# Kernel tuning notes

Hardware: AMD Instinct MI355X
Metric: run time of the kernel (lower is better)

## Reference

```python
import jax, jax.numpy as jnp
import numpy as np

HEAD = 128
E = 1536
MAXPOS = 2048

def _rope_tables(seq_len, d):
    # get_sinusoid_encoding_table: col 2i = sin(pos/10000^(2i/d)), col 2i+1 = cos(same)
    pos = np.arange(seq_len, dtype=np.float32)[:, None]
    i = np.arange(d // 2, dtype=np.float32)
    ang = pos / np.power(10000.0, 2.0 * i / d)  # [seq, d/2]
    cos_pos = np.repeat(np.cos(ang), 2, axis=-1)  # table[:,1::2] repeat_interleave(2)
    sin_pos = np.repeat(np.sin(ang), 2, axis=-1)  # table[:,0::2] repeat_interleave(2)
    return jnp.asarray(cos_pos), jnp.asarray(sin_pos)

def _apply_rope(x, cos_pos, sin_pos):
    # x: [b, s, d]; rotate pairs (x0,x1) -> (-x1, x0)
    x2 = jnp.stack([-x[..., 1::2], x[..., ::2]], axis=-1).reshape(x.shape)
    return x * cos_pos + x2 * sin_pos

def setup_inputs() -> dict:
    key = jax.random.key(0)
    ks = jax.random.split(key, 6)
    b, s, h = 4, 2048, 768
    return {
        "hidden_states": jax.random.normal(ks[0], (b, s, h), jnp.float32),
        "attention_mask": jnp.ones((b, 1, 1, s), jnp.float32),
        "Wi": jax.random.normal(ks[1], (h, 2 * E + HEAD), jnp.float32) * 0.02,
        "bi": jnp.zeros((2 * E + HEAD,), jnp.float32),
        "gamma": 1.0 + jax.random.normal(ks[2], (2, HEAD), jnp.float32) * 0.02,
        "beta": jnp.zeros((2, HEAD), jnp.float32),
        "Wo": jax.random.normal(ks[3], (E, h), jnp.float32) * 0.02,
        "bo": jnp.zeros((h,), jnp.float32),
    }

def reference(hidden_states, attention_mask, Wi, bi, gamma, beta, Wo, bo):
    b, s, _ = hidden_states.shape
    x = jax.nn.silu(hidden_states @ Wi + bi)  # hidden_act='swish'
    u, v, qk = jnp.split(x, [E, 2 * E], axis=-1)  # [b,s,E],[b,s,E],[b,s,HEAD]
    # OffsetScale with 2 heads -> q, k
    q = qk * gamma[0] + beta[0]
    k = qk * gamma[1] + beta[1]
    cos_pos, sin_pos = _rope_tables(s, HEAD)
    q = _apply_rope(q, cos_pos, sin_pos)
    k = _apply_rope(k, cos_pos, sin_pos)
    scores = jnp.einsum('bid,bjd->bij', q, k) / jnp.sqrt(jnp.float32(HEAD))
    add_mask = (1.0 - attention_mask) * -1e12  # [b,1,1,s]
    scores = scores + jnp.squeeze(add_mask, axis=1)  # broadcast [b,1,s]
    # softmax_plus normalization
    valid = (scores > -1e11).astype(scores.dtype)
    l = jnp.maximum(jnp.sum(valid, axis=-1, keepdims=True), 1.0)
    scale = jnp.log(l) / jnp.log(jnp.float32(512.0))
    attn = jax.nn.softmax(scores * scale, axis=-1)
    out = (u * jnp.einsum('bij,bjd->bid', attn, v)) @ Wo + bo
    return out
```

## Files before the change

### kernel.cpp

```cpp
#include <hip/hip_runtime.h>
#include <math.h>

typedef _Float16 f16;
typedef _Float16 f16x8 __attribute__((ext_vector_type(8)));
typedef float f32x4 __attribute__((ext_vector_type(4)));

#define HEAD 128
#define EDIM 1536
#define NI   3200
#define NIP  3328
#define HDIM 768
#define BATCH 4
#define SEQ  2048
#define MTOT (BATCH*SEQ)

__device__ __forceinline__ void gld_lds16(const void* g, void* l) {
  __builtin_amdgcn_global_load_lds(
      (const __attribute__((address_space(1))) void*)g,
      (__attribute__((address_space(3))) void*)l, 16, 0, 0);
}

__global__ __launch_bounds__(256) void cast_f32_f16_k(const float* __restrict__ in,
                                                      f16* __restrict__ out, int n4) {
  int i = blockIdx.x * 256 + threadIdx.x;
  if (i >= n4) return;
  float4 x = ((const float4*)in)[i];
  union { f16 h[4]; short4 s; } u;
  u.h[0] = (f16)x.x; u.h[1] = (f16)x.y; u.h[2] = (f16)x.z; u.h[3] = (f16)x.w;
  ((short4*)out)[i] = u.s;
}

__global__ __launch_bounds__(256) void transpose_cast_k(const float* __restrict__ in, int ld_in,
                                                        f16* __restrict__ out, int ld_out) {
  __shared__ float tile[32][33];
  int c = threadIdx.x & 31, r0 = threadIdx.x >> 5;
  int ib = blockIdx.y * 32, jb = blockIdx.x * 32;
#pragma unroll
  for (int rr = 0; rr < 32; rr += 8)
    tile[r0 + rr][c] = in[(size_t)(ib + r0 + rr) * ld_in + jb + c];
  __syncthreads();
#pragma unroll
  for (int rr = 0; rr < 32; rr += 8)
    out[(size_t)(jb + r0 + rr) * ld_out + ib + c] = (f16)tile[c][r0 + rr];
}

__global__ __launch_bounds__(256) void rope_tables_k(float* __restrict__ cosT,
                                                     float* __restrict__ sinT) {
  int id = blockIdx.x * 256 + threadIdx.x;
  int pos = id >> 6, i = id & 63;
  float ang = (float)pos / powf(10000.0f, (float)(2 * i) / 128.0f);
  float cv = cosf(ang), sv = sinf(ang);
  cosT[pos * HEAD + 2 * i]     = cv;
  cosT[pos * HEAD + 2 * i + 1] = cv;
  sinT[pos * HEAD + 2 * i]     = sv;
  sinT[pos * HEAD + 2 * i + 1] = sv;
}

__global__ __launch_bounds__(256) void addmask_k(const float* __restrict__ mask,
                                                 float* __restrict__ am) {
  int i = blockIdx.x * 256 + threadIdx.x;
  am[i] = (1.0f - mask[i]) * -1e12f;
}

__global__ __launch_bounds__(256) void rope_gate_k(const f16* __restrict__ qkraw,
                                                   const float* __restrict__ gamma,
                                                   const float* __restrict__ beta,
                                                   const float* __restrict__ cosT,
                                                   const float* __restrict__ sinT,
                                                   f16* __restrict__ Qh,
                                                   f16* __restrict__ Kh) {
  int id = blockIdx.x * 256 + threadIdx.x;
  int row = id >> 4, c0i = (id & 15) * 8;
  int pos = row & (SEQ - 1);
  f16x8 sv8 = *(const f16x8*)(qkraw + (size_t)row * HEAD + c0i);
  f16 oq[8], ok[8];
#pragma unroll
  for (int e = 0; e < 8; e += 2) {
    int c = c0i + e;
    float cs = cosT[pos * HEAD + c], sn = sinT[pos * HEAD + c];
    float s0 = (float)sv8[e], s1 = (float)sv8[e + 1];
    float q0 = s0 * gamma[c] + beta[c];
    float q1 = s1 * gamma[c + 1] + beta[c + 1];
    oq[e]     = (f16)(q0 * cs - q1 * sn);
    oq[e + 1] = (f16)(q1 * cs + q0 * sn);
    float k0 = s0 * gamma[128 + c] + beta[128 + c];
    float k1 = s1 * gamma[128 + c + 1] + beta[128 + c + 1];
    ok[e]     = (f16)(k0 * cs - k1 * sn);
    ok[e + 1] = (f16)(k1 * cs + k0 * sn);
  }
  *(f16x8*)(Qh + (size_t)row * HEAD + c0i) = *(f16x8*)oq;
  *(f16x8*)(Kh + (size_t)row * HEAD + c0i) = *(f16x8*)ok;
}

template <int MODE>
__global__ __launch_bounds__(512, 2)
void gemm8p(const f16* __restrict__ A, int lda,
            const f16* __restrict__ B0, int ldb, long long sB, int bshift, int K,
            f16* __restrict__ outH, f16* __restrict__ outH2,
            f16* __restrict__ outV,
            const float* __restrict__ c0, const f16* __restrict__ hA) {
  __shared__ f16 LS[2][2][2][2][4096];
  int bx, by;
  {
    int gx = gridDim.x;
    int id = blockIdx.y * gx + blockIdx.x;
    int cpx = (gx * gridDim.y) >> 3;
    int sw = (id & 7) * cpx + (id >> 3);
    bx = sw % gx; by = sw / gx;
  }
  const int m0 = by * 256, n0 = bx * 256;
  const int t = threadIdx.x;
  const int lane = t & 63, w = t >> 6;
  const int wr = w >> 2, wc = w & 3;
  const int lr = lane & 15, kg = lane >> 4;
  const int bb = by >> bshift;
  const f16* Bb = B0 + (size_t)bb * sB;

  const int rb = t >> 3;
  const int sl = ((t & 7) ^ (rb & 7)) << 3;
  const f16* gA = A  + (size_t)(m0 + rb) * lda + sl;
  const f16* gB = Bb + (size_t)(n0 + rb) * ldb + sl;
  char* lA = (char*)LS + w * 1024;
  char* lB = (char*)LS + 32768 + w * 1024;

  auto stageA = [&](int kt, int h) {
    const f16* s = gA + (size_t)(h << 7) * lda + (kt << 6);
    char* d = lA + ((kt & 1) << 16) + (h << 14);
    gld_lds16(s, d);
    gld_lds16(s + ((size_t)lda << 6), d + 8192);
  };
  auto stageB = [&](int kt, int h) {
    const f16* s = gB + (size_t)(h << 7) * ldb + (kt << 6);
    char* d = lB + ((kt & 1) << 16) + (h << 14);
    gld_lds16(s, d);
    gld_lds16(s + ((size_t)ldb << 6), d + 8192);
  };

  const char* RA = (const char*)LS + ((wr * 128 + lr) << 7);
  const char* RB = (const char*)LS + 32768 + ((wc * 64 + lr) << 7);
  const int sw0 = (kg ^ (lr & 7)) << 4;
  const int sw1 = ((4 + kg) ^ (lr & 7)) << 4;

  f32x4 acc[8][4];
#pragma unroll
  for (int i = 0; i < 8; ++i)
#pragma unroll
    for (int j = 0; j < 4; ++j) acc[i][j] = f32x4{0.f, 0.f, 0.f, 0.f};

  const int nt = K >> 6;
  stageA(0, 0); stageA(0, 1); stageB(0, 0); stageB(0, 1);
  asm volatile("" ::: "memory");
  if (nt > 1) {
    stageB(1, 0); stageB(1, 1);
    asm volatile("s_waitcnt vmcnt(4)" ::: "memory");
  } else {
    asm volatile("s_waitcnt vmcnt(0)" ::: "memory");
  }
  __builtin_amdgcn_s_barrier();
  asm volatile("" ::: "memory");

  for (int tt = 0; tt < nt; ++tt) {
    const char* SA = RA + ((tt & 1) << 16);
    const char* SB = RB + ((tt & 1) << 16);
    f16x8 a0[4][2], a1[4][2], b0[2][2], b1[2][2];
#pragma unroll
    for (int i2 = 0; i2 < 4; ++i2) {
      a0[i2][0] = *(const f16x8*)(SA + (i2 << 11) + sw0);
      a0[i2][1] = *(const f16x8*)(SA + (i2 << 11) + sw1);
    }
#pragma unroll
    for (int j2 = 0; j2 < 2; ++j2) {
      b0[j2][0] = *(const f16x8*)(SB + (j2 << 11) + sw0);
      b0[j2][1] = *(const f16x8*)(SB + (j2 << 11) + sw1);
    }
    if (tt + 1 < nt) stageA(tt + 1, 0);
    __builtin_amdgcn_s_barrier();
    asm volatile("" ::: "memory");
    __builtin_amdgcn_s_setprio(1);
#pragma unroll
    for (int ks = 0; ks < 2; ++ks)
#pragma unroll
      for (int i2 = 0; i2 < 4; ++i2)
#pragma unroll
        for (int j2 = 0; j2 < 2; ++j2)
          acc[i2][j2] = __builtin_amdgcn_mfma_f32_16x16x32_f16(
              a0[i2][ks], b0[j2][ks], acc[i2][j2], 0, 0, 0);
    __builtin_amdgcn_s_setprio(0);
    __builtin_amdgcn_s_barrier();
    asm volatile("" ::: "memory");
#pragma unroll
    for (int j2 = 0; j2 < 2; ++j2) {
      b1[j2][0] = *(const f16x8*)(SB + ((2 + j2) << 11) + sw0);
      b1[j2][1] = *(const f16x8*)(SB + ((2 + j2) << 11) + sw1);
    }
    if (tt + 1 < nt) stageA(tt + 1, 1);
    __builtin_amdgcn_s_barrier();
    asm volatile("" ::: "memory");
    __builtin_amdgcn_s_setprio(1);
#pragma unroll
    for (int ks = 0; ks < 2; ++ks)
#pragma unroll
      for (int i2 = 0; i2 < 4; ++i2)
#pragma unroll
        for (int j2 = 0; j2 < 2; ++j2)
          acc[i2][2 + j2] = __builtin_amdgcn_mfma_f32_16x16x32_f16(
              a0[i2][ks], b1[j2][ks], acc[i2][2 + j2], 0, 0, 0);
    __builtin_amdgcn_s_setprio(0);
    __builtin_amdgcn_s_barrier();
    asm volatile("" ::: "memory");
#pragma unroll
    for (int i2 = 0; i2 < 4; ++i2) {
      a1[i2][0] = *(const f16x8*)(SA + ((4 + i2) << 11) + sw0);
      a1[i2][1] = *(const f16x8*)(SA + ((4 + i2) << 11) + sw1);
    }
    if (tt + 2 < nt) stageB(tt + 2, 0);
    __builtin_amdgcn_s_barrier();
    asm volatile("" ::: "memory");
    __builtin_amdgcn_s_setprio(1);
#pragma unroll
    for (int ks = 0; ks < 2; ++ks)
#pragma unroll
      for (int i2 = 0; i2 < 4; ++i2)
#pragma unroll
        for (int j2 = 0; j2 < 2; ++j2)
          acc[4 + i2][j2] = __builtin_amdgcn_mfma_f32_16x16x32_f16(
              a1[i2][ks], b0[j2][ks], acc[4 + i2][j2], 0, 0, 0);
    __builtin_amdgcn_s_setprio(0);
    __builtin_amdgcn_s_barrier();
    asm volatile("" ::: "memory");
    if (tt + 2 < nt) stageB(tt + 2, 1);
    __builtin_amdgcn_s_barrier();
    asm volatile("" ::: "memory");
    __builtin_amdgcn_s_setprio(1);
#pragma unroll
    for (int ks = 0; ks < 2; ++ks)
#pragma unroll
      for (int i2 = 0; i2 < 4; ++i2)
#pragma unroll
        for (int j2 = 0; j2 < 2; ++j2)
          acc[4 + i2][2 + j2] = __builtin_amdgcn_mfma_f32_16x16x32_f16(
              a1[i2][ks], b1[j2][ks], acc[4 + i2][2 + j2], 0, 0, 0);
    __builtin_amdgcn_s_setprio(0);
    if (tt + 2 < nt) asm volatile("s_waitcnt vmcnt(4)" ::: "memory");
    else             asm volatile("s_waitcnt vmcnt(0)" ::: "memory");
    __builtin_amdgcn_s_barrier();
    asm volatile("" ::: "memory");
  }

  if (MODE == 2) {
    const int colbase = n0 + wc * 64;
#pragma unroll
    for (int i = 0; i < 8; ++i)
#pragma unroll
      for (int j = 0; j < 4; ++j)
#pragma unroll
        for (int r = 0; r < 4; ++r) {
          int row = m0 + wr * 128 + i * 16 + kg * 4 + r;
          int col = colbase + j * 16 + lr;
          float uu = (float)hA[(size_t)row * EDIM + col];
          outH[(size_t)row * EDIM + col] = (f16)(acc[i][j][r] * uu);
        }
    return;
  }
  if (MODE == 1 && bx == 12) {
    const int colbase = n0 + wc * 64;
    if (colbase >= 3200) return;
#pragma unroll
    for (int i = 0; i < 8; ++i)
#pragma unroll
      for (int j = 0; j < 4; ++j)
#pragma unroll
        for (int r = 0; r < 4; ++r) {
          int row = m0 + wr * 128 + i * 16 + kg * 4 + r;
          int col = colbase + j * 16 + lr;
          float xb = acc[i][j][r] + c0[col];
          float s = xb * __builtin_amdgcn_rcpf(1.0f + __expf(-xb));
          outH2[row * HEAD + (col - 3072)] = (f16)s;
        }
    return;
  }
  f16* OT = (f16*)LS;
#pragma unroll
  for (int i = 0; i < 8; ++i) {
#pragma unroll
    for (int j = 0; j < 4; ++j) {
#pragma unroll
      for (int r = 0; r < 4; ++r) {
        int row = wr * 128 + i * 16 + kg * 4 + r;
        int col = wc * 64 + j * 16 + lr;
        float xb = acc[i][j][r] + c0[n0 + col];
        f16 v = (f16)(xb * __builtin_amdgcn_rcpf(1.0f + __expf(-xb)));
        int slot = ((col >> 3) ^ (row & 7) ^ ((row >> 3) & 7));
        OT[row * 256 + ((slot << 3) | (col & 7))] = v;
      }
    }
  }
  __syncthreads();
  if (bx < 6) {
    const int tr = t >> 3, tc = t & 7;
#pragma unroll
    for (int rp = 0; rp < 4; ++rp) {
#pragma unroll
      for (int cc = 0; cc < 4; ++cc) {
        int row = rp * 64 + tr;
        int cIdx = cc * 8 + tc;
        int slot = (cIdx ^ (row & 7) ^ ((row >> 3) & 7));
        f16x8 vv = *(const f16x8*)&OT[row * 256 + (slot << 3)];
        *(f16x8*)&outH[(size_t)(m0 + row) * EDIM + n0 + cIdx * 8] = vv;
      }
    }
  } else {
    f16* Vtb = outV + (size_t)(by >> 3) * EDIM * SEQ;
    const int vbase = n0 - EDIM;
    const int rib0 = m0 & (SEQ - 1);
    const int rg = t & 31;
    const int cw = t >> 5;
    const int fm = ((cw & 1) << 2) | ((cw >> 1) & 3) | ((cw >> 3) << 3);
#pragma unroll
    for (int it = 0; it < 16; ++it) {
      int c = it * 16 + fm;
      f16 seg[8];
#pragma unroll
      for (int e = 0; e < 8; ++e) {
        int row = rg * 8 + e;
        int slot = ((c >> 3) ^ (row & 7) ^ ((row >> 3) & 7));
        seg[e] = OT[row * 256 + ((slot << 3) | (c & 7))];
      }
      *(f16x8*)&Vtb[(size_t)(vbase + c) * SEQ + rib0 + rg * 8] = *(f16x8*)seg;
    }
  }
}

__global__ __launch_bounds__(256, 2)
void scores_os(const f16* __restrict__ Q, const f16* __restrict__ Kt,
               f16* __restrict__ P, const float* __restrict__ am) {
  __shared__ f16 Qs[128 * 128];
  __shared__ f16 Ks[128 * 128];
  const int z = blockIdx.z;
  const int m0 = blockIdx.y * 128, n0 = blockIdx.x * 128;
  const int t = threadIdx.x;
  const int lane = t & 63, w = t >> 6;
  const int wr = w >> 1, wc = w & 1;
  const int lr = lane & 15, kg = lane >> 4;

  const f16* Qb = Q  + (size_t)z * SEQ * HEAD;
  const f16* Kb = Kt + (size_t)z * SEQ * HEAD;

  const int rq = t >> 4, l = t & 15;
#pragma unroll
  for (int c = 0; c < 8; ++c) {
    int row = c * 16 + rq;
    int lq = l ^ (row & 15);
    gld_lds16(Qb + (size_t)(m0 + row) * HEAD + lq * 8, (char*)Qs + c * 4096 + w * 1024);
    gld_lds16(Kb + (size_t)(n0 + row) * HEAD + lq * 8, (char*)Ks + c * 4096 + w * 1024);
  }
  asm volatile("s_waitcnt vmcnt(0)" ::: "memory");
  __syncthreads();

  f32x4 acc[4][4];
#pragma unroll
  for (int i = 0; i < 4; ++i)
#pragma unroll
    for (int j = 0; j < 4; ++j) acc[i][j] = f32x4{0.f, 0.f, 0.f, 0.f};

#pragma unroll
  for (int kk = 0; kk < 4; ++kk) {
    f16x8 af[4], bf[4];
#pragma unroll
    for (int i = 0; i < 4; ++i) {
      int rA = wr * 64 + i * 16 + lr;
      af[i] = *(const f16x8*)&Qs[rA * 128 + (((kk * 4 + kg) ^ (rA & 15)) << 3)];
      int rB = wc * 64 + i * 16 + lr;
      bf[i] = *(const f16x8*)&Ks[rB * 128 + (((kk * 4 + kg) ^ (rB & 15)) << 3)];
    }
#pragma unroll
    for (int i = 0; i < 4; ++i)
#pragma unroll
      for (int j = 0; j < 4; ++j)
        acc[i][j] = __builtin_amdgcn_mfma_f32_16x16x32_f16(af[i], bf[j], acc[i][j], 0, 0, 0);
  }

  f16* outP = P + (size_t)z * SEQ * SEQ;
  const float* c = am + (size_t)z * SEQ;
#pragma unroll
  for (int i = 0; i < 4; ++i)
#pragma unroll
    for (int j = 0; j < 4; ++j)
#pragma unroll
      for (int r = 0; r < 4; ++r) {
        int row = m0 + wr * 64 + i * 16 + kg * 4 + r;
        int col = n0 + wc * 64 + j * 16 + lr;
        outP[(size_t)row * SEQ + col] = (f16)(acc[i][j][r] * 0.08838834764831845f + c[col]);
      }
}

__global__ __launch_bounds__(256, 4)
void gemm_final(const f16* __restrict__ A, int lda,
                const f16* __restrict__ Bt, int ldb, int K,
                float* __restrict__ outF, const float* __restrict__ c0) {
  __shared__ f16 As0[128 * 32], As1[128 * 32], Bs0[128 * 32], Bs1[128 * 32];
  int bx, by;
  {
    int gx = gridDim.x;
    int id = blockIdx.y * gx + blockIdx.x;
    int cpx = (gx * gridDim.y) >> 3;
    int sw = (id & 7) * cpx + (id >> 3);
    bx = sw % gx; by = sw / gx;
  }
  const int m0 = by * 128, n0 = bx * 128;
  const int t = threadIdx.x;
  const int lane = t & 63, w = t >> 6;
  const int wr = w >> 1, wc = w & 1;
  const int lr = lane & 15, kg = lane >> 4;

  const f16* ga = A  + (size_t)(m0 + (t >> 2)) * lda + (t & 3) * 8;
  const f16* gb = Bt + (size_t)(n0 + (t >> 2)) * ldb + (t & 3) * 8;

  f32x4 acc[4][4];
#pragma unroll
  for (int i = 0; i < 4; ++i)
#pragma unroll
    for (int j = 0; j < 4; ++j) acc[i][j] = f32x4{0.f, 0.f, 0.f, 0.f};

  auto stage = [&](f16* AS, f16* BS, int kk) {
    gld_lds16(ga + kk,                    (char*)AS + w * 1024);
    gld_lds16(ga + (size_t)64 * lda + kk, (char*)AS + w * 1024 + 4096);
    gld_lds16(gb + kk,                    (char*)BS + w * 1024);
    gld_lds16(gb + (size_t)64 * ldb + kk, (char*)BS + w * 1024 + 4096);
  };
  auto compute = [&](const f16* AS, const f16* BS) {
    f16x8 af[4], bf[4];
#pragma unroll
    for (int i = 0; i < 4; ++i) {
      af[i] = *(const f16x8*)&AS[(wr * 64 + i * 16 + lr) * 32 + kg * 8];
      bf[i] = *(const f16x8*)&BS[(wc * 64 + i * 16 + lr) * 32 + kg * 8];
    }
#pragma unroll
    for (int i = 0; i < 4; ++i)
#pragma unroll
      for (int j = 0; j < 4; ++j)
        acc[i][j] = __builtin_amdgcn_mfma_f32_16x16x32_f16(af[i], bf[j], acc[i][j], 0, 0, 0);
  };

  stage(As0, Bs0, 0);
  __syncthreads();
  for (int k0 = 0; k0 < K; k0 += 64) {
    if (k0 + 32 < K) stage(As1, Bs1, k0 + 32);
    compute(As0, Bs0);
    __syncthreads();
    if (k0 + 64 < K) stage(As0, Bs0, k0 + 64);
    compute(As1, Bs1);
    __syncthreads();
  }

#pragma unroll
  for (int i = 0; i < 4; ++i)
#pragma unroll
    for (int j = 0; j < 4; ++j)
#pragma unroll
      for (int r = 0; r < 4; ++r) {
        int row = m0 + wr * 64 + i * 16 + kg * 4 + r;
        int col = n0 + wc * 64 + j * 16 + lr;
        outF[(size_t)row * HDIM + col] = acc[i][j][r] + c0[col];
      }
}

__global__ __launch_bounds__(256) void softmax_plus_f16(f16* __restrict__ P) {
  __shared__ float red[4];
  const int t = threadIdx.x;
  f16* pr = P + (size_t)blockIdx.x * SEQ;
  union { uint4 u4; f16 h[8]; } ld;
  ld.u4 = ((const uint4*)pr)[t];
  float v[8];
#pragma unroll
  for (int i = 0; i < 8; ++i) v[i] = fmaxf((float)ld.h[i], -1e12f);

  float cnt = 0.f;
#pragma unroll
  for (int i = 0; i < 8; ++i) cnt += (v[i] > -1e11f) ? 1.0f : 0.0f;
#pragma unroll
  for (int o = 32; o; o >>= 1) cnt += __shfl_xor(cnt, o, 64);
  if ((t & 63) == 0) red[t >> 6] = cnt;
  __syncthreads();
  cnt = red[0] + red[1] + red[2] + red[3];
  float scale = __logf(fmaxf(cnt, 1.0f)) * 0.16025848f;

  float mx = -INFINITY;
#pragma unroll
  for (int i = 0; i < 8; ++i) { v[i] *= scale; mx = fmaxf(mx, v[i]); }
#pragma unroll
  for (int o = 32; o; o >>= 1) mx = fmaxf(mx, __shfl_xor(mx, o, 64));
  __syncthreads();
  if ((t & 63) == 0) red[t >> 6] = mx;
  __syncthreads();
  mx = fmaxf(fmaxf(red[0], red[1]), fmaxf(red[2], red[3]));

  float p[8], sum = 0.f;
#pragma unroll
  for (int i = 0; i < 8; ++i) { p[i] = __expf(v[i] - mx); sum += p[i]; }
#pragma unroll
  for (int o = 32; o; o >>= 1) sum += __shfl_xor(sum, o, 64);
  __syncthreads();
  if ((t & 63) == 0) red[t >> 6] = sum;
  __syncthreads();
  sum = red[0] + red[1] + red[2] + red[3];
  float inv = __builtin_amdgcn_rcpf(sum);

  union { f16 h[8]; uint4 u4; } pk;
#pragma unroll
  for (int i = 0; i < 8; ++i) pk.h[i] = (f16)(p[i] * inv);
  ((uint4*)pr)[t] = pk.u4;
}

extern "C" void kernel_launch(void* const* d_in, const int* in_sizes, int n_in,
                              void* d_out, int out_size, void* d_ws, size_t ws_size,
                              hipStream_t stream) {
  const float* hs    = (const float*)d_in[0];
  const float* mask  = (const float*)d_in[1];
  const float* Wi    = (const float*)d_in[2];
  const float* bi    = (const float*)d_in[3];
  const float* gamma = (const float*)d_in[4];
  const float* beta  = (const float*)d_in[5];
  const float* Wo    = (const float*)d_in[6];
  const float* bo    = (const float*)d_in[7];
  float* out = (float*)d_out;

  const int nb = (ws_size >= ((size_t)160 << 20)) ? BATCH : 1;

  char* p = (char*)d_ws;
  auto alloc = [&](size_t b) { char* r = p; p += (b + 255) & ~(size_t)255; return r; };
  f16*   Xh    = (f16*)  alloc((size_t)MTOT * EDIM * 2);
  f16*   Vt    = (f16*)  alloc((size_t)BATCH * EDIM * SEQ * 2);
  f16*   qkraw = (f16*)  alloc((size_t)MTOT * HEAD * 2);
  f16*   Qh    = (f16*)  alloc((size_t)MTOT * HEAD * 2);
  f16*   Kh    = (f16*)  alloc((size_t)MTOT * HEAD * 2);
  f16*   Ah    = (f16*)  alloc((size_t)MTOT * HDIM * 2);
  f16*   WiT   = (f16*)  alloc((size_t)NIP * HDIM * 2);
  f16*   WoT   = (f16*)  alloc((size_t)HDIM * EDIM * 2);
  float* cosT  = (float*)alloc((size_t)SEQ * HEAD * 4);
  float* sinT  = (float*)alloc((size_t)SEQ * HEAD * 4);
  float* am    = (float*)alloc((size_t)BATCH * SEQ * 4);
  f16*   G     = (f16*)  alloc((size_t)MTOT * EDIM * 2);
  f16*   P     = (f16*)  alloc((size_t)nb * SEQ * SEQ * 2);

  cast_f32_f16_k<<<dim3(MTOT * HDIM / 4 / 256), 256, 0, stream>>>(hs, Ah, MTOT * HDIM / 4);
  transpose_cast_k<<<dim3(NI / 32, HDIM / 32), 256, 0, stream>>>(Wi, NI, WiT, HDIM);
  transpose_cast_k<<<dim3(HDIM / 32, EDIM / 32), 256, 0, stream>>>(Wo, HDIM, WoT, EDIM);
  rope_tables_k<<<dim3(SEQ * 64 / 256), 256, 0, stream>>>(cosT, sinT);
  addmask_k<<<dim3(BATCH * SEQ / 256), 256, 0, stream>>>(mask, am);

  gemm8p<1><<<dim3(NIP / 256, MTOT / 256), 512, 0, stream>>>(
      Ah, HDIM, WiT, HDIM, 0, 30, HDIM,
      Xh, qkraw, Vt, bi, nullptr);
  rope_gate_k<<<dim3(MTOT * 16 / 256), 256, 0, stream>>>(
      qkraw, gamma, beta, cosT, sinT, Qh, Kh);

  const int bsh = (nb == BATCH) ? 3 : 30;
  for (int b0 = 0; b0 < BATCH; b0 += nb) {
    scores_os<<<dim3(SEQ / 128, SEQ / 128, nb), 256, 0, stream>>>(
        Qh + (size_t)b0 * SEQ * HEAD, Kh + (size_t)b0 * SEQ * HEAD,
        P, am + b0 * SEQ);
    softmax_plus_f16<<<dim3(nb * SEQ), 256, 0, stream>>>(P);
    gemm8p<2><<<dim3(EDIM / 256, nb * SEQ / 256), 512, 0, stream>>>(
        P, SEQ, Vt + (size_t)b0 * EDIM * SEQ, SEQ, (long long)EDIM * SEQ, bsh, SEQ,
        G + (size_t)b0 * SEQ * EDIM, nullptr, nullptr, nullptr,
        Xh + (size_t)b0 * SEQ * EDIM);
  }

  gemm_final<<<dim3(HDIM / 128, MTOT / 128), 256, 0, stream>>>(
      G, EDIM, WoT, EDIM, EDIM, out, bo);
}
```

Baseline: 204.7 us.

## Add dedicated 256x128 BK32 GEMM for input projection, drop N padding

```diff
diff --git a/kernel.cpp b/kernel.cpp
--- a/kernel.cpp
+++ b/kernel.cpp
@@ -8,7 +8,6 @@
 #define HEAD 128
 #define EDIM 1536
 #define NI   3200
-#define NIP  3328
 #define HDIM 768
 #define BATCH 4
 #define SEQ  2048
@@ -92,14 +91,11 @@
   *(f16x8*)(Kh + (size_t)row * HEAD + c0i) = *(f16x8*)ok;
 }
 
-template <int MODE>
-__global__ __launch_bounds__(512, 2)
-void gemm8p(const f16* __restrict__ A, int lda,
-            const f16* __restrict__ B0, int ldb, long long sB, int bshift, int K,
-            f16* __restrict__ outH, f16* __restrict__ outH2,
-            f16* __restrict__ outV,
-            const float* __restrict__ c0, const f16* __restrict__ hA) {
-  __shared__ f16 LS[2][2][2][2][4096];
+__global__ __launch_bounds__(512, 4)
+void gemm1_bk32(const f16* __restrict__ A, const f16* __restrict__ Bt,
+                f16* __restrict__ outH, f16* __restrict__ qkout,
+                f16* __restrict__ outV, const float* __restrict__ c0) {
+  __shared__ f16 LS[24576];
   int bx, by;
   {
     int gx = gridDim.x;
@@ -108,6 +104,148 @@
     int sw = (id & 7) * cpx + (id >> 3);
     bx = sw % gx; by = sw / gx;
   }
+  const int m0 = by * 256, n0 = bx * 128;
+  const int t = threadIdx.x;
+  const int lane = t & 63, w = t >> 6;
+  const int wr = w >> 1, wc = w & 1;
+  const int lr = lane & 15, kg = lane >> 4;
+
+  const int rs = t >> 2;
+  const int ssw = ((t & 3) ^ (rs & 3) ^ ((rs >> 2) & 3));
+  const f16* gA = A  + (size_t)(m0 + rs) * HDIM + ssw * 8;
+  const f16* gB = Bt + (size_t)(n0 + rs) * HDIM + ssw * 8;
+
+  auto stage = [&](int kt) {
+    int b = kt & 1;
+    const f16* sa = gA + kt * 32;
+    char* da = (char*)LS + b * 16384 + w * 1024;
+    gld_lds16(sa, da);
+    gld_lds16(sa + (size_t)128 * HDIM, da + 8192);
+    gld_lds16(gB + kt * 32, (char*)LS + 32768 + b * 8192 + w * 1024);
+  };
+
+  f32x4 acc[4][4];
+#pragma unroll
+  for (int i = 0; i < 4; ++i)
+#pragma unroll
+    for (int j = 0; j < 4; ++j) acc[i][j] = f32x4{0.f, 0.f, 0.f, 0.f};
+
+  const int nt = HDIM / 32;
+  stage(0); stage(1);
+  asm volatile("s_waitcnt vmcnt(3)" ::: "memory");
+  __builtin_amdgcn_s_barrier();
+  asm volatile("" ::: "memory");
+
+  for (int tt = 0; tt < nt; ++tt) {
+    const f16* SA = LS + (tt & 1) * 8192;
+    const f16* SB = LS + 16384 + (tt & 1) * 4096;
+    f16x8 a[4], b[4];
+#pragma unroll
+    for (int i = 0; i < 4; ++i) {
+      int rA = wr * 64 + i * 16 + lr;
+      a[i] = *(const f16x8*)&SA[rA * 32 + ((kg ^ (rA & 3) ^ ((rA >> 2) & 3)) << 3)];
+      int rB = wc * 64 + i * 16 + lr;
+      b[i] = *(const f16x8*)&SB[rB * 32 + ((kg ^ (rB & 3) ^ ((rB >> 2) & 3)) << 3)];
+    }
+    asm volatile("s_waitcnt lgkmcnt(0)" ::: "memory");
+    __builtin_amdgcn_s_barrier();
+    asm volatile("" ::: "memory");
+    if (tt + 2 < nt) stage(tt + 2);
+    __builtin_amdgcn_s_setprio(1);
+#pragma unroll
+    for (int i = 0; i < 4; ++i)
+#pragma unroll
+      for (int j = 0; j < 4; ++j)
+        acc[i][j] = __builtin_amdgcn_mfma_f32_16x16x32_f16(a[i], b[j], acc[i][j], 0, 0, 0);
+    __builtin_amdgcn_s_setprio(0);
+    if (tt + 2 < nt) asm volatile("s_waitcnt vmcnt(3)" ::: "memory");
+    else             asm volatile("s_waitcnt vmcnt(0)" ::: "memory");
+    __builtin_amdgcn_s_barrier();
+    asm volatile("" ::: "memory");
+  }
+
+  if (bx == 24) {
+#pragma unroll
+    for (int i = 0; i < 4; ++i)
+#pragma unroll
+      for (int j = 0; j < 4; ++j)
+#pragma unroll
+        for (int r = 0; r < 4; ++r) {
+          int row = m0 + wr * 64 + i * 16 + kg * 4 + r;
+          int col = n0 + wc * 64 + j * 16 + lr;
+          float xb = acc[i][j][r] + c0[col];
+          float s = xb * __builtin_amdgcn_rcpf(1.0f + __expf(-xb));
+          qkout[row * HEAD + (col - 3072)] = (f16)s;
+        }
+    return;
+  }
+  f16* OT = LS;
+  for (int h = 0; h < 2; ++h) {
+    if ((wr >> 1) == h) {
+#pragma unroll
+      for (int i = 0; i < 4; ++i)
+#pragma unroll
+        for (int j = 0; j < 4; ++j)
+#pragma unroll
+          for (int r = 0; r < 4; ++r) {
+            int rw = (wr & 1) * 64 + i * 16 + kg * 4 + r;
+            int col = wc * 64 + j * 16 + lr;
+            float xb = acc[i][j][r] + c0[n0 + col];
+            f16 v = (f16)(xb * __builtin_amdgcn_rcpf(1.0f + __expf(-xb)));
+            int slot = ((col >> 3) ^ (rw & 7) ^ ((rw >> 3) & 7)) & 15;
+            OT[rw * 128 + slot * 8 + (col & 7)] = v;
+          }
+    }
+    __syncthreads();
+    if (bx < 12) {
+      const int tr = t >> 3, tc = t & 7;
+#pragma unroll
+      for (int rp = 0; rp < 2; ++rp) {
+#pragma unroll
+        for (int cc = 0; cc < 2; ++cc) {
+          int rw = rp * 64 + tr;
+          int cIdx = cc * 8 + tc;
+          int slot = (cIdx ^ (rw & 7) ^ ((rw >> 3) & 7)) & 15;
+          f16x8 vv = *(const f16x8*)&OT[rw * 128 + slot * 8];
+          *(f16x8*)&outH[(size_t)(m0 + h * 128 + rw) * EDIM + n0 + cIdx * 8] = vv;
+        }
+      }
+    } else {
+      f16* Vtb = outV + (size_t)(by >> 3) * EDIM * SEQ;
+      const int vbase = n0 - EDIM;
+      const int rib0 = (m0 & (SEQ - 1)) + h * 128;
+      const int rg = t & 15, cw = t >> 4;
+#pragma unroll
+      for (int it = 0; it < 4; ++it) {
+        int c = it * 32 + cw;
+        f16 seg[8];
+#pragma unroll
+        for (int e = 0; e < 8; ++e) {
+          int rw = rg * 8 + e;
+          int slot = ((c >> 3) ^ (rw & 7) ^ ((rw >> 3) & 7)) & 15;
+          seg[e] = OT[rw * 128 + slot * 8 + (c & 7)];
+        }
+        *(f16x8*)&Vtb[(size_t)(vbase + c) * SEQ + rib0 + rg * 8] = *(f16x8*)seg;
+      }
+    }
+    __syncthreads();
+  }
+}
+
+template <int MODE>
+__global__ __launch_bounds__(512, 2)
+void gemm8p(const f16* __restrict__ A, int lda,
+            const f16* __restrict__ B0, int ldb, long long sB, int bshift, int K,
+            f16* __restrict__ outH, const f16* __restrict__ hA) {
+  __shared__ f16 LSL[2][2][2][2][4096];
+  int bx, by;
+  {
+    int gx = gridDim.x;
+    int id = blockIdx.y * gx + blockIdx.x;
+    int cpx = (gx * gridDim.y) >> 3;
+    int sw = (id & 7) * cpx + (id >> 3);
+    bx = sw % gx; by = sw / gx;
+  }
   const int m0 = by * 256, n0 = bx * 256;
   const int t = threadIdx.x;
   const int lane = t & 63, w = t >> 6;
@@ -120,8 +258,8 @@
   const int sl = ((t & 7) ^ (rb & 7)) << 3;
   const f16* gA = A  + (size_t)(m0 + rb) * lda + sl;
   const f16* gB = Bb + (size_t)(n0 + rb) * ldb + sl;
-  char* lA = (char*)LS + w * 1024;
-  char* lB = (char*)LS + 32768 + w * 1024;
+  char* lA = (char*)LSL + w * 1024;
+  char* lB = (char*)LSL + 32768 + w * 1024;
 
   auto stageA = [&](int kt, int h) {
     const f16* s = gA + (size_t)(h << 7) * lda + (kt << 6);
@@ -136,8 +274,8 @@
     gld_lds16(s + ((size_t)ldb << 6), d + 8192);
   };
 
-  const char* RA = (const char*)LS + ((wr * 128 + lr) << 7);
-  const char* RB = (const char*)LS + 32768 + ((wc * 64 + lr) << 7);
+  const char* RA = (const char*)LSL + ((wr * 128 + lr) << 7);
+  const char* RB = (const char*)LSL + 32768 + ((wc * 64 + lr) << 7);
   const int sw0 = (kg ^ (lr & 7)) << 4;
   const int sw1 = ((4 + kg) ^ (lr & 7)) << 4;
 
@@ -247,88 +385,18 @@
     asm volatile("" ::: "memory");
   }
 
-  if (MODE == 2) {
-    const int colbase = n0 + wc * 64;
-#pragma unroll
-    for (int i = 0; i < 8; ++i)
-#pragma unroll
-      for (int j = 0; j < 4; ++j)
-#pragma unroll
-        for (int r = 0; r < 4; ++r) {
-          int row = m0 + wr * 128 + i * 16 + kg * 4 + r;
-          int col = colbase + j * 16 + lr;
-          float uu = (float)hA[(size_t)row * EDIM + col];
-          outH[(size_t)row * EDIM + col] = (f16)(acc[i][j][r] * uu);
-        }
-    return;
-  }
-  if (MODE == 1 && bx == 12) {
-    const int colbase = n0 + wc * 64;
-    if (colbase >= 3200) return;
-#pragma unroll
-    for (int i = 0; i < 8; ++i)
-#pragma unroll
-      for (int j = 0; j < 4; ++j)
-#pragma unroll
-        for (int r = 0; r < 4; ++r) {
-          int row = m0 + wr * 128 + i * 16 + kg * 4 + r;
-          int col = colbase + j * 16 + lr;
-          float xb = acc[i][j][r] + c0[col];
-          float s = xb * __builtin_amdgcn_rcpf(1.0f + __expf(-xb));
-          outH2[row * HEAD + (col - 3072)] = (f16)s;
-        }
-    return;
-  }
-  f16* OT = (f16*)LS;
-#pragma unroll
-  for (int i = 0; i < 8; ++i) {
-#pragma unroll
-    for (int j = 0; j < 4; ++j) {
+  const int colbase = n0 + wc * 64;
+#pragma unroll
+  for (int i = 0; i < 8; ++i)
+#pragma unroll
+    for (int j = 0; j < 4; ++j)
 #pragma unroll
       for (int r = 0; r < 4; ++r) {
-        int row = wr * 128 + i * 16 + kg * 4 + r;
-        int col = wc * 64 + j * 16 + lr;
-        float xb = acc[i][j][r] + c0[n0 + col];
-        f16 v = (f16)(xb * __builtin_amdgcn_rcpf(1.0f + __expf(-xb)));
-        int slot = ((col >> 3) ^ (row & 7) ^ ((row >> 3) & 7));
-        OT[row * 256 + ((slot << 3) | (col & 7))] = v;
+        int row = m0 + wr * 128 + i * 16 + kg * 4 + r;
+        int col = colbase + j * 16 + lr;
+        float uu = (float)hA[(size_t)row * EDIM + col];
+        outH[(size_t)row * EDIM + col] = (f16)(acc[i][j][r] * uu);
       }
-    }
-  }
-  __syncthreads();
-  if (bx < 6) {
-    const int tr = t >> 3, tc = t & 7;
-#pragma unroll
-    for (int rp = 0; rp < 4; ++rp) {
-#pragma unroll
-      for (int cc = 0; cc < 4; ++cc) {
-        int row = rp * 64 + tr;
-        int cIdx = cc * 8 + tc;
-        int slot = (cIdx ^ (row & 7) ^ ((row >> 3) & 7));
-        f16x8 vv = *(const f16x8*)&OT[row * 256 + (slot << 3)];
-        *(f16x8*)&outH[(size_t)(m0 + row) * EDIM + n0 + cIdx * 8] = vv;
-      }
-    }
-  } else {
-    f16* Vtb = outV + (size_t)(by >> 3) * EDIM * SEQ;
-    const int vbase = n0 - EDIM;
-    const int rib0 = m0 & (SEQ - 1);
-    const int rg = t & 31;
-    const int cw = t >> 5;
-    const int fm = ((cw & 1) << 2) | ((cw >> 1) & 3) | ((cw >> 3) << 3);
-#pragma unroll
-    for (int it = 0; it < 16; ++it) {
-      int c = it * 16 + fm;
-      f16 seg[8];
-#pragma unroll
-      for (int e = 0; e < 8; ++e) {
-        int row = rg * 8 + e;
-        int slot = ((c >> 3) ^ (row & 7) ^ ((row >> 3) & 7));
-        seg[e] = OT[row * 256 + ((slot << 3) | (c & 7))];
-      }
-      *(f16x8*)&Vtb[(size_t)(vbase + c) * SEQ + rib0 + rg * 8] = *(f16x8*)seg;
-    }
-  }
 }
 
 __global__ __launch_bounds__(256, 2)
@@ -535,7 +603,7 @@
   f16*   Qh    = (f16*)  alloc((size_t)MTOT * HEAD * 2);
   f16*   Kh    = (f16*)  alloc((size_t)MTOT * HEAD * 2);
   f16*   Ah    = (f16*)  alloc((size_t)MTOT * HDIM * 2);
-  f16*   WiT   = (f16*)  alloc((size_t)NIP * HDIM * 2);
+  f16*   WiT   = (f16*)  alloc((size_t)NI * HDIM * 2);
   f16*   WoT   = (f16*)  alloc((size_t)HDIM * EDIM * 2);
   float* cosT  = (float*)alloc((size_t)SEQ * HEAD * 4);
   float* sinT  = (float*)alloc((size_t)SEQ * HEAD * 4);
@@ -549,9 +617,8 @@
   rope_tables_k<<<dim3(SEQ * 64 / 256), 256, 0, stream>>>(cosT, sinT);
   addmask_k<<<dim3(BATCH * SEQ / 256), 256, 0, stream>>>(mask, am);
 
-  gemm8p<1><<<dim3(NIP / 256, MTOT / 256), 512, 0, stream>>>(
-      Ah, HDIM, WiT, HDIM, 0, 30, HDIM,
-      Xh, qkraw, Vt, bi, nullptr);
+  gemm1_bk32<<<dim3(NI / 128, MTOT / 256), 512, 0, stream>>>(
+      Ah, WiT, Xh, qkraw, Vt, bi);
   rope_gate_k<<<dim3(MTOT * 16 / 256), 256, 0, stream>>>(
       qkraw, gamma, beta, cosT, sinT, Qh, Kh);
 
@@ -563,7 +630,7 @@
     softmax_plus_f16<<<dim3(nb * SEQ), 256, 0, stream>>>(P);
     gemm8p<2><<<dim3(EDIM / 256, nb * SEQ / 256), 512, 0, stream>>>(
         P, SEQ, Vt + (size_t)b0 * EDIM * SEQ, SEQ, (long long)EDIM * SEQ, bsh, SEQ,
-        G + (size_t)b0 * SEQ * EDIM, nullptr, nullptr, nullptr,
+        G + (size_t)b0 * SEQ * EDIM,
         Xh + (size_t)b0 * SEQ * EDIM);
   }
 
```

Result: slower. 290.1 us (+41.7%).
